# Kernel tuning notes

Hardware: AMD Instinct MI355X
Metric: run time of the kernel (lower is better)

Reference implementation:

```python
import jax, jax.numpy as jnp
import numpy as np

C_LOGIT = 10.0  # logit clipping constant C from __init__
NEG_INF = -1e8


def setup_inputs() -> dict:
    key = jax.random.key(0)
    ks = jax.random.split(key, 10)
    B, S, E, H = 512, 256, 128, 128
    u = lambda k, sh: jax.random.uniform(k, sh, jnp.float32, -0.1, 0.1)
    return {
        "low_context_vector": jax.random.normal(ks[0], (B, S, E), jnp.float32),
        "original_node": jax.random.uniform(ks[1], (S, 2), jnp.float32),
        "mask": jnp.zeros((B, S), jnp.float32),
        # learned parameters
        "low_init_w": jax.random.uniform(ks[2], (2 * E,), jnp.float32, -1.0, 1.0),
        "Wc": u(ks[3], (E, E)),   "bc": u(ks[4], (E,)),     # low_h_context_embed
        "Wv": u(ks[5], (2 * E, E)), "bv": u(ks[6], (E,)),   # low_v_weight_embed
        "Wq": u(ks[7], (E, H)),                              # pointer query proj
        "Wref": u(ks[8], (E, H)),                            # pointer ref proj
        "v": u(ks[9], (H,)),                                 # pointer score vector
    }


def _decode(cv, mask, low_init_w, Wc, bc, Wv, bv, Wq, Wref, v, key):
    B, S, E = cv.shape
    h_bar = jnp.mean(cv, axis=1) @ Wc + bc              # [B,E]
    rest0 = low_init_w @ Wv + bv                        # [E]
    query0 = h_bar + rest0[None, :]                     # [B,E]
    ref = cv @ Wref                                     # [B,S,H], hoisted out of loop
    mask = mask.at[:, 0].set(1.0)                       # start node visited
    keys = jax.random.split(key, S - 1)
    binds = jnp.arange(B)

    def step(carry, k):
        mask, query, init_h, i = carry
        u_ = jnp.tanh((query @ Wq)[:, None, :] + ref) @ v      # [B,S]
        logits = jnp.where(mask > 0, NEG_INF, C_LOGIT * jnp.tanh(u_))
        logp = jax.nn.log_softmax(logits, axis=-1)
        g = jax.random.gumbel(k, logits.shape, logits.dtype)
        idx = jnp.argmax(logits + g, axis=-1)                  # Categorical sample, [B]
        lp = jnp.take_along_axis(logp, idx[:, None], axis=1)[:, 0]
        mask = mask.at[binds, idx].set(1.0)
        h = cv[binds, idx]                                     # gathered embedding [B,E]
        init_h = jnp.where(i == 0, h, init_h)                  # first pick cached
        query = h_bar + (jnp.concatenate([init_h, h], axis=-1) @ Wv + bv)
        return (mask, query, init_h, i + 1), (idx, lp)

    init = (mask, query0, jnp.zeros((B, E), cv.dtype), jnp.int32(0))
    _, (idxs, lps) = jax.lax.scan(step, init, keys)
    return idxs.T, lps.T  # [B, S-1] each


def reference(low_context_vector, original_node, mask, low_init_w, Wc, bc, Wv, bv, Wq, Wref, v):
    # original_node only feeds a printed local_reward in the torch code; it does
    # not affect the returned (indices, log_probs), so it is unused here.
    return _decode(low_context_vector, mask, low_init_w, Wc, bc, Wv, bv, Wq, Wref, v,
                   jax.random.key(42))
```

## Files before the change

kernel.cpp:

```cpp
#include <hip/hip_runtime.h>
#include <hip/hip_bf16.h>
#include <stdint.h>
#include <math.h>

#define NBATCH 512
#define NS 256
#define NE 128
#define NH 128
#define NSTEPS 255
#define NEGINF -1e8f
#define SENT_NEG -1e30f

__device__ __forceinline__ uint32_t rotl32(uint32_t x, uint32_t r) {
  return (x << r) | (x >> (32u - r));
}

__device__ __forceinline__ void tf2x32(uint32_t k0, uint32_t k1,
                                       uint32_t x0, uint32_t x1,
                                       uint32_t& o0, uint32_t& o1) {
  uint32_t ks2 = k0 ^ k1 ^ 0x1BD11BDAu;
  x0 += k0; x1 += k1;
#define TF_R4(a,b,c,d) \
  x0 += x1; x1 = rotl32(x1,a); x1 ^= x0; \
  x0 += x1; x1 = rotl32(x1,b); x1 ^= x0; \
  x0 += x1; x1 = rotl32(x1,c); x1 ^= x0; \
  x0 += x1; x1 = rotl32(x1,d); x1 ^= x0;
  TF_R4(13,15,26,6)   x0 += k1;  x1 += ks2 + 1u;
  TF_R4(17,29,16,24)  x0 += ks2; x1 += k0 + 2u;
  TF_R4(13,15,26,6)   x0 += k0;  x1 += k1 + 3u;
  TF_R4(17,29,16,24)  x0 += k1;  x1 += ks2 + 4u;
  TF_R4(13,15,26,6)   x0 += ks2; x1 += k0 + 5u;
#undef TF_R4
  o0 = x0; o1 = x1;
}

__device__ __forceinline__ float gumbel_of(uint2 key, uint32_t j) {
  uint32_t o0, o1;
  tf2x32(key.x, key.y, 0u, j, o0, o1);
  uint32_t bits = o0 ^ o1;
  float f = __uint_as_float((bits >> 9) | 0x3f800000u) - 1.0f;
  float u = (f == 0.0f) ? 1.17549435e-38f : f;
  float l1 = -logf(u);
  return -logf(l1);
}

__device__ __forceinline__ float nr_tanh(float x) {
  const float Chi = 2.8853900432586670f;
  const float Clo = 3.8519259822379735e-08f;
  float m = fmaf(x, Chi, x * Clo);
  m = fminf(m, 126.0f);
  float tt = __builtin_amdgcn_exp2f(m);
  float d  = tt + 1.0f;
  float r  = __builtin_amdgcn_rcpf(d);
  r = r * fmaf(-d, r, 2.0f);
  return fmaf(-2.0f, r, 1.0f);
}

__device__ __forceinline__ double dot32(const float4* __restrict__ a,
                                        const float4* __restrict__ bp) {
  double s = 0.0;
#pragma unroll
  for (int q = 0; q < 8; ++q) {
    float4 x = a[q], y = bp[q];
    s += (double)x.x * (double)y.x + (double)x.y * (double)y.y
       + (double)x.z * (double)y.z + (double)x.w * (double)y.w;
  }
  return s;
}

__device__ __forceinline__ double dot4d(float4 a, float4 b) {
  return ((double)a.x * (double)b.x + (double)a.y * (double)b.y)
       + ((double)a.z * (double)b.z + (double)a.w * (double)b.w);
}

__global__ void k1_mats(const float* __restrict__ Wv, const float* __restrict__ Wq,
                        const float* __restrict__ liw, const float* __restrict__ bvv,
                        float* __restrict__ M1T, float* __restrict__ M2T,
                        float* __restrict__ rest0) {
  int e = blockIdx.x, h = threadIdx.x;
  __shared__ float wrow[NE];
  if (e < 256) {
    wrow[h] = Wv[e * NE + h];
    __syncthreads();
    double a = 0.0;
    for (int k = 0; k < NE; ++k) a += (double)wrow[k] * (double)Wq[k * NH + h];
    if (e < 128) M1T[h * NE + e] = (float)a;
    else         M2T[h * NE + (e - 128)] = (float)a;
  } else {
    double a = 0.0;
    for (int k = 0; k < 2 * NE; ++k) a += (double)liw[k] * (double)Wv[k * NE + h];
    rest0[h] = (float)a + bvv[h];
  }
}

__global__ void k2_base(const float* __restrict__ cv, const float* __restrict__ Wc,
                        const float* __restrict__ bc, const float* __restrict__ bvv,
                        const float* __restrict__ Wq, const float* __restrict__ rest0,
                        double* __restrict__ qqbase, float* __restrict__ qq0) {
  int b = blockIdx.x, h = threadIdx.x;
  int b256 = b << 8;
  __shared__ float meanL[NE], hbarL[NE];
  double ms = 0.0;
  for (int s = 0; s < NS; ++s) ms += (double)cv[((size_t)b256 + s) * NE + h];
  meanL[h] = (float)(ms * (1.0 / 256.0));
  __syncthreads();
  double a = 0.0;
  for (int e = 0; e < NE; ++e) a += (double)meanL[e] * (double)Wc[e * NE + h];
  hbarL[h] = (float)a + bc[h];
  __syncthreads();
  double ab = 0.0, a0 = 0.0;
  for (int k = 0; k < NE; ++k) {
    double w = (double)Wq[k * NH + h];
    ab += (double)(hbarL[k] + bvv[k]) * w;
    a0 += (double)(hbarL[k] + rest0[k]) * w;
  }
  qqbase[(size_t)b * NH + h] = ab;
  qq0[(size_t)b * NH + h] = (float)a0;
}

__global__ __launch_bounds__(256, 4)
void k_a2v3(const float* __restrict__ cv, const float* __restrict__ M2T,
            double* __restrict__ A2) {
  const int b  = blockIdx.x >> 3;
  const int s0 = (blockIdx.x & 7) << 5;
  const int t  = threadIdx.x;
  const int h  = t >> 1;
  const int kh = t & 1;
  const int b256 = b << 8;
  __shared__ float cvS[32][132];
  for (int idx = t; idx < 32 * NE; idx += 256) {
    int r = idx >> 7, c = idx & 127;
    cvS[r][c] = cv[((size_t)(b256 + s0 + r)) * NE + c];
  }
  __syncthreads();
  float4 m2r[16];
  {
    const float4* m2p = (const float4*)(M2T + (size_t)h * NE + kh * 64);
#pragma unroll
    for (int q = 0; q < 16; ++q) m2r[q] = m2p[q];
  }
#pragma unroll 2
  for (int sLoc = 0; sLoc < 32; ++sLoc) {
    const float4* cr4 = ((const float4*)&cvS[sLoc][0]) + kh * 16;
    double c0 = 0.0, c1 = 0.0;
#pragma unroll
    for (int q = 0; q < 16; q += 2) {
      c0 += dot4d(cr4[q],     m2r[q]);
      c1 += dot4d(cr4[q + 1], m2r[q + 1]);
    }
    double s = c0 + c1;
    s += __shfl_xor(s, 1, 64);
    if (kh == 0)
      A2[((size_t)(b256 + s0 + sLoc)) * NH + h] = s;
  }
}

struct MainSh1 {
  alignas(16) float  qq[NH];
  alignas(16) float  vvf[NH];
  float  logitArr[NS];
  alignas(8)  double base128[NH];
  uint2  keyL[NSTEPS];
  float  redV[2][8];
  float  redS[2][8];
  int    redI[2][8];
  alignas(16) float refScr[2][NE];
  int    sRowId[2];
};

struct PreSh {
  float cvS[NS][33];
  float wS[32][NH];
};

__global__ __launch_bounds__(512, 4)
void decode_1b(const float* __restrict__ cv,
               const float* __restrict__ mask_in,
               const float* __restrict__ Wref,
               const float* __restrict__ vvec,
               const double* __restrict__ qqbase,
               const float* __restrict__ M1T,
               const float* __restrict__ qq0,
               const double* __restrict__ A2,
               float* __restrict__ out) {
  const int b = blockIdx.x;
  const int t = threadIdx.x;
  const int b256 = b << 8;
  const int w = t >> 6, l = t & 63;
  const int i = (w << 5) | (l >> 1);
  const int hHalf = l & 1;
  const int hb = hHalf << 6;
  const int h0 = l << 1;

  __shared__ union { PreSh pre; MainSh1 m; } sh;
  __shared__ short rowId0[NS];
  __shared__ int tmp8[4], nActSh0;

  bool act0 = false; int preCnt = 0;
  if (t < NS) {
    act0 = !((t == 0) || (mask_in[(size_t)b256 + t] > 0.0f));
    uint64_t mb = __ballot(act0);
    int lane = t & 63, wv = t >> 6;
    preCnt = __popcll(mb & (((uint64_t)1 << lane) - 1));
    if (lane == 0) tmp8[wv] = (int)__popcll(mb);
  }
  __syncthreads();
  if (t < NS && act0) {
    int base = 0;
    for (int k = 0; k < (t >> 6); ++k) base += tmp8[k];
    rowId0[base + preCnt] = (short)t;
  }
  if (t == 0) nActSh0 = tmp8[0] + tmp8[1] + tmp8[2] + tmp8[3];
  __syncthreads();
  const int nAct0 = nActSh0;

  int myRow = (i < nAct0) ? (int)rowId0[i] : 0;
  float refr[64];
#pragma unroll
  for (int j = 0; j < 64; ++j) refr[j] = 0.0f;

  for (int ec = 0; ec < 4; ++ec) {
    __syncthreads();
    for (int ii = t; ii < 32 * NH; ii += 512) {
      int r = ii >> 7, c = ii & 127;
      sh.pre.wS[r][c] = Wref[(ec * 32 + r) * NH + c];
    }
    for (int ii = t; ii < NS * 32; ii += 512) {
      int r = ii >> 5, c = ii & 31;
      sh.pre.cvS[r][c] = cv[((size_t)b256 + r) * NE + ec * 32 + c];
    }
    __syncthreads();
    for (int hc = 0; hc < 8; ++hc) {
      double a[8] = {0,0,0,0,0,0,0,0};
      for (int e = 0; e < 32; ++e) {
        double cd = (double)sh.pre.cvS[myRow][e];
        const float* wp = &sh.pre.wS[e][hb + hc * 8];
#pragma unroll
        for (int j = 0; j < 8; ++j) a[j] += cd * (double)wp[j];
      }
#pragma unroll
      for (int j = 0; j < 8; ++j) refr[hc * 8 + j] += (float)a[j];
    }
  }
  __syncthreads();

  if (t < NSTEPS) {
    uint32_t o0, o1;
    tf2x32(0u, 42u, 0u, (uint32_t)t, o0, o1);
    sh.m.keyL[t] = make_uint2(o0, o1);
  }
  if (t < NH) {
    sh.m.vvf[t] = vvec[t];
    sh.m.qq[t] = qq0[(size_t)b * NH + t];
  }
  __syncthreads();

  float g = 0.0f;
  if (i < nAct0)
    g = gumbel_of(sh.m.keyL[0], (uint32_t)(b256 + myRow));
  bool adoptNext = false;

  for (int step = 0; step < NSTEPS; ++step) {
    const int par = step & 1;
    const int nA = nAct0 - step;
    const bool active = (i < nA);

    if (adoptNext) {
      myRow = sh.m.sRowId[par ^ 1];
      const float4* rs4 = (const float4*)(&sh.m.refScr[par ^ 1][hb]);
#pragma unroll
      for (int q = 0; q < 16; ++q) {
        float4 v4 = rs4[q];
        refr[4 * q + 0] = v4.x; refr[4 * q + 1] = v4.y;
        refr[4 * q + 2] = v4.z; refr[4 * q + 3] = v4.w;
      }
      adoptNext = false;
    }
    if (active && i == nA - 1) {
      float4* rs4 = (float4*)(&sh.m.refScr[par][hb]);
#pragma unroll
      for (int q = 0; q < 16; ++q)
        rs4[q] = make_float4(refr[4 * q + 0], refr[4 * q + 1],
                             refr[4 * q + 2], refr[4 * q + 3]);
      sh.m.sRowId[par] = myRow;
    }

    double accH = 0.0;
    if (active) {
      double a0 = 0, a1 = 0, a2 = 0, a3 = 0;
      const float4* qq4 = (const float4*)(sh.m.qq + hb);
      const float4* vv4 = (const float4*)(sh.m.vvf + hb);
#pragma unroll
      for (int q = 0; q < 16; ++q) {
        float4 qv = qq4[q];
        float4 wv = vv4[q];
        a0 += (double)nr_tanh(qv.x + refr[4 * q + 0]) * (double)wv.x;
        a1 += (double)nr_tanh(qv.y + refr[4 * q + 1]) * (double)wv.y;
        a2 += (double)nr_tanh(qv.z + refr[4 * q + 2]) * (double)wv.z;
        a3 += (double)nr_tanh(qv.w + refr[4 * q + 3]) * (double)wv.w;
      }
      accH = (a0 + a1) + (a2 + a3);
    }
    double other = __shfl_xor(accH, 1, 64);
    float val = SENT_NEG; int bR = 0x7fffffff; float term = 0.0f;
    if (active) {
      double tot = hHalf ? (other + accH) : (accH + other);
      float u_ = (float)tot;
      float logit = 10.0f * (float)tanh((double)u_);
      if (!hHalf) {
        sh.m.logitArr[myRow] = logit;
        term = expf(logit);
      }
      val = logit + g;
      bR = myRow;
    }

    float bvv = val; float bss = term;
#pragma unroll
    for (int mm = 1; mm <= 32; mm <<= 1) {
      float ov = __shfl_xor(bvv, mm, 64);
      int   oR = __shfl_xor(bR,  mm, 64);
      float os = __shfl_xor(bss, mm, 64);
      bss += os;
      if (ov > bvv || (ov == bvv && oR < bR)) { bvv = ov; bR = oR; }
    }

    const bool waveNext = ((w << 5) < nA - 1) && (step + 1 < NSTEPS);

    double pf0 = 0.0, pf1 = 0.0; bool havePf = false;
    if (waveNext && step > 0 && (unsigned)bR <= 255u) {
      const double* ap = A2 + (size_t)(b256 + bR) * NH + h0;
      pf0 = ap[0]; pf1 = ap[1]; havePf = true;
    }

    if (l == 0) {
      sh.m.redV[par][w] = bvv; sh.m.redI[par][w] = bR; sh.m.redS[par][w] = bss;
    }
    __syncthreads();

    float BV = sh.m.redV[par][0]; int BR_ = sh.m.redI[par][0];
#pragma unroll
    for (int k = 1; k < 8; ++k) {
      float ov = sh.m.redV[par][k]; int oR = sh.m.redI[par][k];
      if (ov > BV || (ov == BV && oR < BR_)) { BV = ov; BR_ = oR; }
    }
    if ((unsigned)BR_ > 255u) BR_ = 0;
    const int BI = BR_;

    if (t == 0) {
      float SS = (sh.m.redS[par][0] + sh.m.redS[par][1]) + (sh.m.redS[par][2] + sh.m.redS[par][3]);
      SS += (sh.m.redS[par][4] + sh.m.redS[par][5]) + (sh.m.redS[par][6] + sh.m.redS[par][7]);
      float lp = sh.m.logitArr[BI] - (float)log((double)SS);
      out[(size_t)b * NSTEPS + step] = (float)BI;
      out[(size_t)NBATCH * NSTEPS + (size_t)b * NSTEPS + step] = lp;
    }

    adoptNext = active && (myRow == BI) && (i != nA - 1);

    if (step + 1 < NSTEPS && i < nA - 1) {
      int ridN = adoptNext ? sh.m.sRowId[par] : myRow;
      g = gumbel_of(sh.m.keyL[step + 1], (uint32_t)(b256 + ridN));
    }

    if (step == 0) {
      if (NSTEPS > 1) {
        const int hq = t >> 2, kq = t & 3;
        const float4* hrow = (const float4*)(cv + (size_t)(b256 + BI) * NE + kq * 32);
        const float4* m1p  = (const float4*)(M1T + (size_t)hq * NE + kq * 32);
        double am = dot32(hrow, m1p);
        am += __shfl_xor(am, 1, 64);
        am += __shfl_xor(am, 2, 64);
        if (kq == 0)
          sh.m.base128[hq] = qqbase[(size_t)b * NH + hq] + am;
        __syncthreads();
        if (waveNext) {
          double a0v = A2[(size_t)(b256 + BI) * NH + h0];
          double a1v = A2[(size_t)(b256 + BI) * NH + h0 + 1];
          sh.m.qq[h0]     = (float)(sh.m.base128[h0]     + a0v);
          sh.m.qq[h0 + 1] = (float)(sh.m.base128[h0 + 1] + a1v);
        }
      }
    } else if (waveNext) {
      double a0v, a1v;
      if (havePf && bR == BI) { a0v = pf0; a1v = pf1; }
      else {
        a0v = A2[(size_t)(b256 + BI) * NH + h0];
        a1v = A2[(size_t)(b256 + BI) * NH + h0 + 1];
      }
      sh.m.qq[h0]     = (float)(sh.m.base128[h0]     + a0v);
      sh.m.qq[h0 + 1] = (float)(sh.m.base128[h0 + 1] + a1v);
    }
  }
}

__device__ __forceinline__ float fast_tanh_ref(float x) {
  const float Chi = 2.8853900432586670f;
  const float Clo = 3.8519259822379735e-08f;
  float m = fmaf(x, Chi, x * Clo);
  float tt = exp2f(m);
  return 1.0f - 2.0f / (tt + 1.0f);
}

struct MainShR {
  float  query[NE];
  float  qq[NH];
  float  hbar[NE];
  float  inith[NE];
  float  hcur[NE];
  alignas(16) double vvd[NH];
  float  logitArr[NS];
  float  maskArr[NS];
  uint2  keyL[NSTEPS];
  float  meanv[NE];
  float  redV[4];
  int    redI[4];
  double redS[4];
  int    idxSh;
};
struct PreShR {
  float cvS[NS][33];
  float wS[32][NH];
};

__global__ __launch_bounds__(256, 2)
void decoder_kernel_ref(const float* __restrict__ cv, const float* __restrict__ mask_in,
                        const float* __restrict__ liw, const float* __restrict__ Wc,
                        const float* __restrict__ bc, const float* __restrict__ Wv,
                        const float* __restrict__ bv, const float* __restrict__ Wq,
                        const float* __restrict__ Wref, const float* __restrict__ vvec,
                        float* __restrict__ out) {
  const int b = blockIdx.x;
  const int t = threadIdx.x;
  const int b256 = b << 8;
  __shared__ union { PreShR pre; MainShR m; } sh;

  float refr[NH];
#pragma unroll
  for (int h = 0; h < NH; ++h) refr[h] = 0.0f;
  for (int ec = 0; ec < 4; ++ec) {
    const int e0 = ec * 32;
    __syncthreads();
    for (int i = t; i < 32 * NH; i += 256) {
      int r = i >> 7, h = i & 127;
      sh.pre.wS[r][h] = Wref[(e0 + r) * NH + h];
    }
    for (int i = t; i < NS * 32; i += 256) {
      int s2 = i >> 5, j = i & 31;
      sh.pre.cvS[s2][j] = cv[((size_t)b256 + s2) * NE + e0 + j];
    }
    __syncthreads();
#pragma unroll
    for (int hc = 0; hc < 16; ++hc) {
      double a[8] = {0,0,0,0,0,0,0,0};
      for (int e = 0; e < 32; ++e) {
        double cd = (double)sh.pre.cvS[t][e];
#pragma unroll
        for (int j = 0; j < 8; ++j) a[j] += cd * (double)sh.pre.wS[e][hc * 8 + j];
      }
#pragma unroll
      for (int j = 0; j < 8; ++j) refr[hc * 8 + j] += (float)a[j];
    }
  }
  __syncthreads();

  if (t < NSTEPS) {
    uint32_t o0, o1;
    tf2x32(0u, 42u, 0u, (uint32_t)t, o0, o1);
    sh.m.keyL[t] = make_uint2(o0, o1);
  }
  if (t < NH) sh.m.vvd[t] = (double)vvec[t];
  sh.m.maskArr[t] = (mask_in[(size_t)b256 + t] > 0.0f || t == 0) ? 1.0f : 0.0f;
  if (t < NE) {
    double s64 = 0.0;
    for (int s2 = 0; s2 < NS; ++s2) s64 += (double)cv[((size_t)b256 + s2) * NE + t];
    sh.m.meanv[t] = (float)(s64 * (1.0 / 256.0));
  }
  __syncthreads();
  if (t < NE) {
    double acc = 0.0;
    for (int e = 0; e < NE; ++e) acc += (double)sh.m.meanv[e] * (double)Wc[e * NE + t];
    float hbv = (float)acc + bc[t];
    sh.m.hbar[t] = hbv;
    double acc2 = 0.0;
    for (int k = 0; k < 2 * NE; ++k) acc2 += (double)liw[k] * (double)Wv[k * NE + t];
    float r0 = (float)acc2 + bv[t];
    sh.m.query[t] = hbv + r0;
  }
  __syncthreads();

  for (int step = 0; step < NSTEPS; ++step) {
    if (t < NH) {
      double acc = 0.0;
      for (int k = 0; k < NE; ++k) acc += (double)sh.m.query[k] * (double)Wq[k * NH + t];
      sh.m.qq[t] = (float)acc;
    }
    __syncthreads();

    float logit;
    bool masked = (sh.m.maskArr[t] != 0.0f);
    if (!masked) {
      double a0 = 0.0, a1 = 0.0, a2 = 0.0, a3 = 0.0;
      const float4*  qq4 = (const float4*)sh.m.qq;
      const double2* vv2 = (const double2*)sh.m.vvd;
#pragma unroll
      for (int h4 = 0; h4 < 32; ++h4) {
        float4  q  = qq4[h4];
        double2 va = vv2[2 * h4];
        double2 vb = vv2[2 * h4 + 1];
        a0 += (double)fast_tanh_ref(q.x + refr[4 * h4 + 0]) * va.x;
        a1 += (double)fast_tanh_ref(q.y + refr[4 * h4 + 1]) * va.y;
        a2 += (double)fast_tanh_ref(q.z + refr[4 * h4 + 2]) * vb.x;
        a3 += (double)fast_tanh_ref(q.w + refr[4 * h4 + 3]) * vb.y;
      }
      float u_ = (float)((a0 + a1) + (a2 + a3));
      logit = 10.0f * (float)tanh((double)u_);
    } else {
      logit = NEGINF;
    }
    sh.m.logitArr[t] = logit;

    uint2 key = sh.m.keyL[step];
    uint32_t j = (uint32_t)(b256 + t);
    uint32_t o0, o1;
    tf2x32(key.x, key.y, 0u, j, o0, o1);
    uint32_t bits = o0 ^ o1;
    float f = __uint_as_float((bits >> 9) | 0x3f800000u) - 1.0f;
    float u = (f == 0.0f) ? 1.17549435e-38f : f;
    float l1 = (float)(-log((double)u));
    float g  = (float)(-log((double)l1));
    float val = logit + g;
    double term = exp((double)logit);

    float bv_ = val; int bi = t; double bs = term;
#pragma unroll
    for (int m = 1; m <= 32; m <<= 1) {
      float  ov = __shfl_xor(bv_, m, 64);
      int    oi = __shfl_xor(bi,  m, 64);
      double os = __shfl_xor(bs,  m, 64);
      if (ov > bv_ || (ov == bv_ && oi < bi)) { bv_ = ov; bi = oi; }
      bs += os;
    }
    int w = t >> 6;
    if ((t & 63) == 0) { sh.m.redV[w] = bv_; sh.m.redI[w] = bi; sh.m.redS[w] = bs; }
    __syncthreads();

    if (t == 0) {
      float BV = sh.m.redV[0]; int BI = sh.m.redI[0];
      for (int k = 1; k < 4; ++k) {
        float ov = sh.m.redV[k]; int oi = sh.m.redI[k];
        if (ov > BV || (ov == BV && oi < BI)) { BV = ov; BI = oi; }
      }
      double SS = ((sh.m.redS[0] + sh.m.redS[1]) + (sh.m.redS[2] + sh.m.redS[3]));
      sh.m.idxSh = BI;
      float lp = sh.m.logitArr[BI] - (float)log(SS);
      out[(size_t)b * NSTEPS + step] = (float)BI;
      out[(size_t)NBATCH * NSTEPS + (size_t)b * NSTEPS + step] = lp;
    }
    __syncthreads();

    int idx = sh.m.idxSh;
    if (t == idx) sh.m.maskArr[t] = 1.0f;
    if (t < NE) {
      float hc = cv[((size_t)b256 + idx) * NE + t];
      sh.m.hcur[t] = hc;
      if (step == 0) sh.m.inith[t] = hc;
    }
    __syncthreads();

    if (t < NE) {
      double acc2 = 0.0;
      for (int k = 0; k < NE; ++k) acc2 += (double)sh.m.inith[k] * (double)Wv[k * NE + t];
      for (int k = 0; k < NE; ++k) acc2 += (double)sh.m.hcur[k] * (double)Wv[(NE + k) * NE + t];
      float mm = (float)acc2 + bv[t];
      sh.m.query[t] = sh.m.hbar[t] + mm;
    }
    __syncthreads();
  }
}

extern "C" void kernel_launch(void* const* d_in, const int* in_sizes, int n_in,
                              void* d_out, int out_size, void* d_ws, size_t ws_size,
                              hipStream_t stream) {
  const float* cv   = (const float*)d_in[0];
  const float* mask = (const float*)d_in[2];
  const float* liw  = (const float*)d_in[3];
  const float* Wc   = (const float*)d_in[4];
  const float* bc   = (const float*)d_in[5];
  const float* Wv   = (const float*)d_in[6];
  const float* bv   = (const float*)d_in[7];
  const float* Wq   = (const float*)d_in[8];
  const float* Wref = (const float*)d_in[9];
  const float* vv   = (const float*)d_in[10];
  (void)in_sizes; (void)n_in; (void)out_size;

  const size_t SZ_QQB = (size_t)NBATCH * NH * sizeof(double);
  const size_t SZ_M   = (size_t)NE * NH * sizeof(float);
  const size_t SZ_QQ0 = (size_t)NBATCH * NH * sizeof(float);
  const size_t SZ_A2  = (size_t)NBATCH * NS * NH * sizeof(double);
  const size_t need_pre = SZ_QQB + 2 * SZ_M + SZ_QQ0 + 512 + SZ_A2;

  if (ws_size >= need_pre) {
    char* p = (char*)d_ws;
    double* qqbase = (double*)p;            p += SZ_QQB;
    float*  M1T    = (float*)p;             p += SZ_M;
    float*  M2T    = (float*)p;             p += SZ_M;
    float*  qq0    = (float*)p;             p += SZ_QQ0;
    float*  rest0  = (float*)p;             p += 512;
    double* A2     = (double*)p;

    k1_mats<<<257, 128, 0, stream>>>(Wv, Wq, liw, bv, M1T, M2T, rest0);
    k2_base<<<NBATCH, 128, 0, stream>>>(cv, Wc, bc, bv, Wq, rest0, qqbase, qq0);
    k_a2v3<<<NBATCH * 8, 256, 0, stream>>>(cv, M2T, A2);
    decode_1b<<<NBATCH, 512, 0, stream>>>(cv, mask, Wref, vv, qqbase, M1T,
                                          qq0, A2, (float*)d_out);
  } else {
    decoder_kernel_ref<<<NBATCH, 256, 0, stream>>>(cv, mask, liw, Wc, bc, Wv, bv,
                                                   Wq, Wref, vv, (float*)d_out);
  }
}
```

Baseline: 3.065 ms.

## Precompute Gumbel noise in a separate kernel and drop speculative A2 prefetch

Adds a kernel that generates all Gumbel noise values into a workspace buffer, so the serial decode loop loads them instead of running threefry hashing and logs on its critical path. It also replaces expf with a hardware exp2 builtin and simplifies the A2 row fetch to happen after the block-wide argmax, removing the speculative per-wave prefetch. The cost is an extra full-grid kernel writing about 134 MB of noise, plus a dependent global load per step. The A2 fetch now waits for the reduction, which may add latency.

```diff
diff --git a/kernel.cpp b/kernel.cpp
--- a/kernel.cpp
+++ b/kernel.cpp
@@ -155,6 +155,15 @@
   }
 }
 
+__global__ __launch_bounds__(256)
+void k_gum(float* __restrict__ G) {
+  const int b = blockIdx.x, step = blockIdx.y, r = threadIdx.x;
+  uint32_t k0, k1;
+  tf2x32(0u, 42u, 0u, (uint32_t)step, k0, k1);
+  float g = gumbel_of(make_uint2(k0, k1), (uint32_t)((b << 8) + r));
+  G[((size_t)b * NSTEPS + step) * NS + r] = g;
+}
+
 struct MainSh1 {
   alignas(16) float  qq[NH];
   alignas(16) float  vvf[NH];
@@ -173,6 +182,7 @@
   float wS[32][NH];
 };
 
+template <int MODEG>
 __global__ __launch_bounds__(512, 4)
 void decode_1b(const float* __restrict__ cv,
                const float* __restrict__ mask_in,
@@ -182,6 +192,7 @@
                const float* __restrict__ M1T,
                const float* __restrict__ qq0,
                const double* __restrict__ A2,
+               const float* __restrict__ G,
                float* __restrict__ out) {
   const int b = blockIdx.x;
   const int t = threadIdx.x;
@@ -191,6 +202,7 @@
   const int hHalf = l & 1;
   const int hb = hHalf << 6;
   const int h0 = l << 1;
+  const float LOG2E = 1.4426950408889634f;
 
   __shared__ union { PreSh pre; MainSh1 m; } sh;
   __shared__ short rowId0[NS];
@@ -256,8 +268,10 @@
   __syncthreads();
 
   float g = 0.0f;
-  if (i < nAct0)
-    g = gumbel_of(sh.m.keyL[0], (uint32_t)(b256 + myRow));
+  if (i < nAct0) {
+    if (MODEG) g = G[((size_t)b * NSTEPS + 0) * NS + myRow];
+    else       g = gumbel_of(sh.m.keyL[0], (uint32_t)(b256 + myRow));
+  }
   bool adoptNext = false;
 
   for (int step = 0; step < NSTEPS; ++step) {
@@ -309,7 +323,7 @@
       float logit = 10.0f * (float)tanh((double)u_);
       if (!hHalf) {
         sh.m.logitArr[myRow] = logit;
-        term = expf(logit);
+        term = __builtin_amdgcn_exp2f(logit * LOG2E);
       }
       val = logit + g;
       bR = myRow;
@@ -324,15 +338,6 @@
       bss += os;
       if (ov > bvv || (ov == bvv && oR < bR)) { bvv = ov; bR = oR; }
     }
-
-    const bool waveNext = ((w << 5) < nA - 1) && (step + 1 < NSTEPS);
-
-    double pf0 = 0.0, pf1 = 0.0; bool havePf = false;
-    if (waveNext && step > 0 && (unsigned)bR <= 255u) {
-      const double* ap = A2 + (size_t)(b256 + bR) * NH + h0;
-      pf0 = ap[0]; pf1 = ap[1]; havePf = true;
-    }
-
     if (l == 0) {
       sh.m.redV[par][w] = bvv; sh.m.redI[par][w] = bR; sh.m.redS[par][w] = bss;
     }
@@ -346,6 +351,14 @@
     }
     if ((unsigned)BR_ > 255u) BR_ = 0;
     const int BI = BR_;
+
+    const bool waveNext = ((w << 5) < nA - 1) && (step + 1 < NSTEPS);
+
+    double a0v = 0.0, a1v = 0.0;
+    if (step > 0 && waveNext) {
+      const double* ap = A2 + (size_t)(b256 + BI) * NH + h0;
+      a0v = ap[0]; a1v = ap[1];
+    }
 
     if (t == 0) {
       float SS = (sh.m.redS[par][0] + sh.m.redS[par][1]) + (sh.m.redS[par][2] + sh.m.redS[par][3]);
@@ -359,7 +372,8 @@
 
     if (step + 1 < NSTEPS && i < nA - 1) {
       int ridN = adoptNext ? sh.m.sRowId[par] : myRow;
-      g = gumbel_of(sh.m.keyL[step + 1], (uint32_t)(b256 + ridN));
+      if (MODEG) g = G[((size_t)b * NSTEPS + (step + 1)) * NS + ridN];
+      else       g = gumbel_of(sh.m.keyL[step + 1], (uint32_t)(b256 + ridN));
     }
 
     if (step == 0) {
@@ -374,19 +388,13 @@
           sh.m.base128[hq] = qqbase[(size_t)b * NH + hq] + am;
         __syncthreads();
         if (waveNext) {
-          double a0v = A2[(size_t)(b256 + BI) * NH + h0];
-          double a1v = A2[(size_t)(b256 + BI) * NH + h0 + 1];
-          sh.m.qq[h0]     = (float)(sh.m.base128[h0]     + a0v);
-          sh.m.qq[h0 + 1] = (float)(sh.m.base128[h0 + 1] + a1v);
+          double b0 = A2[(size_t)(b256 + BI) * NH + h0];
+          double b1 = A2[(size_t)(b256 + BI) * NH + h0 + 1];
+          sh.m.qq[h0]     = (float)(sh.m.base128[h0]     + b0);
+          sh.m.qq[h0 + 1] = (float)(sh.m.base128[h0 + 1] + b1);
         }
       }
     } else if (waveNext) {
-      double a0v, a1v;
-      if (havePf && bR == BI) { a0v = pf0; a1v = pf1; }
-      else {
-        a0v = A2[(size_t)(b256 + BI) * NH + h0];
-        a1v = A2[(size_t)(b256 + BI) * NH + h0 + 1];
-      }
       sh.m.qq[h0]     = (float)(sh.m.base128[h0]     + a0v);
       sh.m.qq[h0 + 1] = (float)(sh.m.base128[h0 + 1] + a1v);
     }
@@ -597,7 +605,9 @@
   const size_t SZ_M   = (size_t)NE * NH * sizeof(float);
   const size_t SZ_QQ0 = (size_t)NBATCH * NH * sizeof(float);
   const size_t SZ_A2  = (size_t)NBATCH * NS * NH * sizeof(double);
+  const size_t SZ_G   = (size_t)NBATCH * NSTEPS * NS * sizeof(float);
   const size_t need_pre = SZ_QQB + 2 * SZ_M + SZ_QQ0 + 512 + SZ_A2;
+  const size_t need_g   = need_pre + SZ_G;
 
   if (ws_size >= need_pre) {
     char* p = (char*)d_ws;
@@ -606,13 +616,20 @@
     float*  M2T    = (float*)p;             p += SZ_M;
     float*  qq0    = (float*)p;             p += SZ_QQ0;
     float*  rest0  = (float*)p;             p += 512;
-    double* A2     = (double*)p;
+    double* A2     = (double*)p;            p += SZ_A2;
+    float*  G      = (float*)p;
 
     k1_mats<<<257, 128, 0, stream>>>(Wv, Wq, liw, bv, M1T, M2T, rest0);
     k2_base<<<NBATCH, 128, 0, stream>>>(cv, Wc, bc, bv, Wq, rest0, qqbase, qq0);
     k_a2v3<<<NBATCH * 8, 256, 0, stream>>>(cv, M2T, A2);
-    decode_1b<<<NBATCH, 512, 0, stream>>>(cv, mask, Wref, vv, qqbase, M1T,
-                                          qq0, A2, (float*)d_out);
+    if (ws_size >= need_g) {
+      k_gum<<<dim3(NBATCH, NSTEPS), 256, 0, stream>>>(G);
+      decode_1b<1><<<NBATCH, 512, 0, stream>>>(cv, mask, Wref, vv, qqbase, M1T,
+                                               qq0, A2, G, (float*)d_out);
+    } else {
+      decode_1b<0><<<NBATCH, 512, 0, stream>>>(cv, mask, Wref, vv, qqbase, M1T,
+                                               qq0, A2, nullptr, (float*)d_out);
+    }
   } else {
     decoder_kernel_ref<<<NBATCH, 256, 0, stream>>>(cv, mask, liw, Wc, bc, Wv, bv,
                                                    Wq, Wref, vv, (float*)d_out);
```

After: 3.019 ms. No clear change (-1.5%).
